# Kernel tuning notes

Measured on AMD Instinct MI355X. Metric: run time of the kernel, lower is better.

## Reference

```python
import jax, jax.numpy as jnp
import numpy as np

# MANO fingertip / palm prior vertex indices from contact_loss
_F1 = [697,698,699,700,712,713,714,715,737,738,739,740,741,743,744,745,746,748,749,750,753,754,755,756,757,758,759,760,761,762,763,764,765,766,767,768]
_F2 = [46,47,48,49,164,165,166,167,194,195,223,237,238,280,281,298,301,317,320,323,324,325,326,327,328,329,330,331,332,333,340,341,342,343,344,345,346,347,348,349,350,351,352,353,354,355]
_F3 = [356,357,358,359,375,376,386,387,396,397,402,403,413,429,433,434,435,436,437,438,439,440,441,442,443,444,452,453,454,455,456,459,460,461,462,463,464,465,466,467]
_F4 = [468,469,470,471,484,485,486,496,497,506,507,513,514,524,545,546,547,548,549,550,551,552,553,555,563,564,565,566,567,570,572,573,574,575,576,577,578]
_F5 = [580,581,582,583,600,601,602,614,615,624,625,630,631,641,663,664,665,666,667,668,670,672,680,681,682,683,684,686,687,688,689,690,691,692,693,694,695]
_F0 = [73,96,98,99,772,774,775,777]
PRIOR_IDX = np.array(_F1 + _F2 + _F3 + _F4 + _F5 + _F0, dtype=np.int32)

KL_COEF = 0.005
A_W, B_W, C_W, D_W, E_W = 1.0, 0.1, 1000.0, 10.0, 10.0  # init kwargs a..e


def _nn(src, trg):
    """Brute-force 1-NN: src [B,N1,3] -> trg [B,N2,3].
    Returns (sq_dist [B,N1], idx [B,N1], diff src-near [B,N1,3])."""
    d2 = (jnp.sum(src * src, -1)[:, :, None]
          + jnp.sum(trg * trg, -1)[:, None, :]
          - 2.0 * jnp.einsum('bnd,bmd->bnm', src, trg))  # [B,N1,N2]
    idx = jnp.argmin(d2, axis=-1)
    near = jnp.take_along_axis(trg, idx[:, :, None], axis=1)
    diff = src - near
    return jnp.sum(diff * diff, axis=-1), idx, diff


def _p2p_signed(x, y, x_normals):
    """point2point_signed(x, y, x_normals): signed dist y->x, unsigned x->y."""
    _, yidx, y2x = _nn(y, x)  # nearest x for each y
    y_nn_normal = jnp.take_along_axis(x_normals, yidx[:, :, None], axis=1)
    in_out = jnp.sign(jnp.sum(y_nn_normal * y2x, axis=-1))
    y2x_signed = jnp.sqrt(jnp.sum(y2x * y2x, axis=-1)) * in_out  # [B,P2]
    _, _, x2y = _nn(x, y)  # nearest y for each x
    x2y_dist = jnp.sqrt(jnp.sum(x2y * x2y, axis=-1))  # [B,P1]
    return y2x_signed, x2y_dist


def _forward(recon_xyz, gt_xyz, recon_normals, gt_normals, obj_xyz, mean, log_var, v_weights):
    B = recon_xyz.shape[0]
    f32 = recon_xyz.dtype
    # --- CVAE recon (L2) + KLD ---
    recon_loss = jnp.sum((recon_xyz - gt_xyz) ** 2) / B
    kld = -0.5 * jnp.sum(1.0 + log_var - mean ** 2 - jnp.exp(log_var)) / B * 10.0
    # --- obj -> hand NN (squared dists, pytorch3d knn_points convention) ---
    recon_d2, recon_idx, _ = _nn(obj_xyz, recon_xyz)  # [B,3000]
    gt_d2, _, _ = _nn(obj_xyz, gt_xyz)
    # --- contact map from GT NN dist thresholding ---
    cmap = jnp.sqrt(gt_d2) < 0.005  # [B,3000] bool
    # --- contact_loss: obj NN to prior (fingertip/palm) recon verts ---
    prior = recon_xyz[:, PRIOR_IDX, :]
    obj_cd, _, _ = _nn(obj_xyz, prior)
    n_pts = jnp.sum(cmap.astype(f32))
    contact = 3000.0 * jnp.where(n_pts > 0, jnp.sum(obj_cd * cmap) / (B * n_pts), 0.0)
    # --- CMap_consistency_loss ---
    recon_cmap = jnp.sqrt(recon_d2) < 0.005
    consistency = -5.0 * jnp.sum((recon_cmap & cmap).astype(f32)) / (n_pts + 1e-4)
    # --- inter_penetr_loss: interior obj points via NN-normal dot sign ---
    nn_hand = jnp.take_along_axis(recon_xyz, recon_idx[:, :, None], axis=1)
    nn_normal = jnp.take_along_axis(recon_normals, recon_idx[:, :, None], axis=1)
    interior = jnp.sum((nn_hand - obj_xyz) * nn_normal, axis=-1) > 0
    penetr = 100.0 * jnp.sum(recon_d2 * interior) / B
    # --- loss_cnet: signed chamfer consistency ---
    vw2 = v_weights ** (1.0 / 2.5)
    o2h, h2o = _p2p_signed(recon_xyz, obj_xyz, recon_normals)
    o2h_gt, h2o_gt = _p2p_signed(gt_xyz, obj_xyz, gt_normals)
    w_dist = (o2h_gt < 0.01) & (o2h_gt > -0.005)
    w_neg = o2h < 0.0
    w = jnp.where(w_neg, 1.5, jnp.where(w_dist, 1.0, 0.1))
    loss_h = 35.0 * (1.0 - KL_COEF) * jnp.mean(jnp.abs(jnp.abs(h2o) - jnp.abs(h2o_gt)) * vw2)
    loss_o = 30.0 * (1.0 - KL_COEF) * jnp.mean(jnp.abs(o2h - o2h_gt) * w)
    cnet = loss_h + loss_o
    return (A_W * recon_loss + B_W * kld + C_W * penetr
            + D_W * contact + E_W * consistency + cnet)


def setup_inputs() -> dict:
    key = jax.random.key(0)
    ks = jax.random.split(key, 8)
    B, NH, NO, Z = 32, 778, 3000, 64
    s = 0.05  # meter-scale point clouds so contact thresholds (5mm) are meaningful
    def unit(k, shape):
        v = jax.random.normal(k, shape, dtype=jnp.float32)
        return v / jnp.linalg.norm(v, axis=-1, keepdims=True)
    return {
        'recon_xyz': jax.random.normal(ks[0], (B, NH, 3), dtype=jnp.float32) * s,
        'gt_xyz': jax.random.normal(ks[1], (B, NH, 3), dtype=jnp.float32) * s,
        'recon_normals': unit(ks[2], (B, NH, 3)),
        'gt_normals': unit(ks[3], (B, NH, 3)),
        'obj_xyz': jax.random.normal(ks[4], (B, NO, 3), dtype=jnp.float32) * s,
        'mean': jax.random.normal(ks[5], (B, Z), dtype=jnp.float32),
        'log_var': jax.random.normal(ks[6], (B, Z), dtype=jnp.float32) * 0.1,
        'v_weights': jax.random.uniform(ks[7], (NH,), dtype=jnp.float32),
    }


def reference(recon_xyz, gt_xyz, recon_normals, gt_normals, obj_xyz, mean, log_var, v_weights):
    return _forward(recon_xyz, gt_xyz, recon_normals, gt_normals, obj_xyz, mean, log_var, v_weights)
```

## Files before the change

kernel.cpp:

```cpp
#include <hip/hip_runtime.h>
#include <math.h>


#define NB 32
#define NH 778
#define NO 3000
#define NZ 64
#define NP 204

#define P_OBJ 4
#define OBJ_PTS (256 * P_OBJ)
#define OBJ_TILES 3
#define JSPLIT 4
#define JCH 195
#define OC_NUM 12
#define OC_SIZE 250

#define OBJ_BLKS (NB * OBJ_TILES * JSPLIT)
#define HAND_BLKS (NB * OC_NUM)
#define FIN_OBJ_BLKS (NB * OBJ_TILES)
#define FIN_TAIL_BLKS ((NB * NH + 255) / 256)
#define FIN_BLKS (FIN_OBJ_BLKS + FIN_TAIL_BLKS)

typedef unsigned int uint32;
typedef unsigned long long ull;

__device__ __constant__ int c_prior[NP] = {
  697,698,699,700,712,713,714,715,737,738,739,740,741,743,744,745,746,748,749,750,
  753,754,755,756,757,758,759,760,761,762,763,764,765,766,767,768,
  46,47,48,49,164,165,166,167,194,195,223,237,238,280,281,298,301,317,320,323,
  324,325,326,327,328,329,330,331,332,333,340,341,342,343,344,345,346,347,348,349,
  350,351,352,353,354,355,
  356,357,358,359,375,376,386,387,396,397,402,403,413,429,433,434,435,436,437,438,
  439,440,441,442,443,444,452,453,454,455,456,459,460,461,462,463,464,465,466,467,
  468,469,470,471,484,485,486,496,497,506,507,513,514,524,545,546,547,548,549,550,
  551,552,553,555,563,564,565,566,567,570,572,573,574,575,576,577,578,
  580,581,582,583,600,601,602,614,615,624,625,630,631,641,663,664,665,666,667,668,
  670,672,680,681,682,683,684,686,687,688,689,690,691,692,693,694,695,
  73,96,98,99,772,774,775,777
};

__device__ inline float wave_sum(float v) {
  v += __shfl_down(v, 32);
  v += __shfl_down(v, 16);
  v += __shfl_down(v, 8);
  v += __shfl_down(v, 4);
  v += __shfl_down(v, 2);
  v += __shfl_down(v, 1);
  return v;
}

#define N_MINH (2 * NB * NH)
#define N_PACK (2 * NB * NO)

__global__ void init_kernel(float* accs, uint32* minH, ull* packO) {
  int t = blockIdx.x * blockDim.x + threadIdx.x;
  if (t < 9) accs[t] = 0.0f;
  if (t < N_MINH) minH[t] = 0x7F800000u;
  if (t < N_PACK) packO[t] = ~0ull;
}

__global__ __launch_bounds__(256) void mega1(
    const float* __restrict__ recon, const float* __restrict__ gt,
    const float* __restrict__ obj,
    uint32* __restrict__ minHR, uint32* __restrict__ minHG,
    ull* __restrict__ packR, ull* __restrict__ packG)
{
  const int bid = blockIdx.x;
  const int tid = threadIdx.x;

  if (bid < OBJ_BLKS) {
    __shared__ float4 sR[JCH];
    __shared__ float4 sG[JCH];
    const int b    = bid / (OBJ_TILES * JSPLIT);
    const int rem  = bid % (OBJ_TILES * JSPLIT);
    const int tile = rem / JSPLIT;
    const int half = rem % JSPLIT;
    const int jbase = half * JCH;
    const int jcnt = (NH - jbase < JCH) ? (NH - jbase) : JCH;

    for (int i = tid; i < jcnt; i += 256) {
      const float* p = recon + ((size_t)b * NH + jbase + i) * 3;
      float x = p[0], y = p[1], z = p[2];
      sR[i] = make_float4(x, y, z, x*x + y*y + z*z);
      const float* q = gt + ((size_t)b * NH + jbase + i) * 3;
      float gx = q[0], gy = q[1], gz = q[2];
      sG[i] = make_float4(gx, gy, gz, gx*gx + gy*gy + gz*gz);
    }
    __syncthreads();

    float nx[P_OBJ], ny[P_OBJ], nz[P_OBJ], o2v[P_OBJ];
    int ob[P_OBJ]; bool val[P_OBJ];
    #pragma unroll
    for (int m = 0; m < P_OBJ; ++m) {
      int o = tile * OBJ_PTS + m * 256 + tid;
      ob[m] = o; val[m] = (o < NO);
      float x = 0.f, y = 0.f, z = 0.f;
      if (val[m]) {
        const float* op = obj + ((size_t)b * NO + o) * 3;
        x = op[0]; y = op[1]; z = op[2];
      }
      nx[m] = -2.f * x; ny[m] = -2.f * y; nz[m] = -2.f * z;
      o2v[m] = x*x + y*y + z*z;
    }

    float bR[P_OBJ], bG[P_OBJ]; int iR[P_OBJ], iG[P_OBJ];
    #pragma unroll
    for (int m = 0; m < P_OBJ; ++m) { bR[m] = 3.4e38f; bG[m] = 3.4e38f; iR[m] = 0; iG[m] = 0; }

    #pragma unroll 2
    for (int i = 0; i < jcnt; ++i) {
      float4 h = sR[i];
      #pragma unroll
      for (int m = 0; m < P_OBJ; ++m) {
        float t = fmaf(nx[m], h.x, h.w);
        t = fmaf(ny[m], h.y, t);
        t = fmaf(nz[m], h.z, t);
        if (t < bR[m]) { bR[m] = t; iR[m] = jbase + i; }
      }
      float4 g = sG[i];
      #pragma unroll
      for (int m = 0; m < P_OBJ; ++m) {
        float u = fmaf(nx[m], g.x, g.w);
        u = fmaf(ny[m], g.y, u);
        u = fmaf(nz[m], g.z, u);
        if (u < bG[m]) { bG[m] = u; iG[m] = jbase + i; }
      }
    }

    #pragma unroll
    for (int m = 0; m < P_OBJ; ++m) {
      if (!val[m]) continue;
      const size_t base = (size_t)b * NO + ob[m];
      float d2R = fmaxf(bR[m] + o2v[m], 0.f);
      float d2G = fmaxf(bG[m] + o2v[m], 0.f);
      atomicMin(&packR[base], ((ull)__float_as_uint(d2R) << 32) | (uint32)iR[m]);
      atomicMin(&packG[base], ((ull)__float_as_uint(d2G) << 32) | (uint32)iG[m]);
    }
  } else {
    __shared__ float4 sO[OC_SIZE];
    const int bid2 = bid - OBJ_BLKS;
    const int oc = bid2 % OC_NUM;
    const int b  = bid2 / OC_NUM;

    const float* Ob = obj + ((size_t)b * NO + oc * OC_SIZE) * 3;
    for (int i = tid; i < OC_SIZE; i += 256) {
      float x = Ob[3*i], y = Ob[3*i+1], z = Ob[3*i+2];
      sO[i] = make_float4(x, y, z, x*x + y*y + z*z);
    }
    __syncthreads();

    float nrx[4], nry[4], nrz[4], r2v[4];
    float ngx[4], ngy[4], ngz[4], g2v[4];
    bool val[4];
    #pragma unroll
    for (int m = 0; m < 4; ++m) {
      int j = m * 256 + tid;
      val[m] = (j < NH);
      float rx = 0.f, ry = 0.f, rz = 0.f, gx = 0.f, gy = 0.f, gz = 0.f;
      if (val[m]) {
        const float* rp = recon + ((size_t)b * NH + j) * 3;
        const float* gp = gt    + ((size_t)b * NH + j) * 3;
        rx = rp[0]; ry = rp[1]; rz = rp[2];
        gx = gp[0]; gy = gp[1]; gz = gp[2];
      }
      nrx[m] = -2.f*rx; nry[m] = -2.f*ry; nrz[m] = -2.f*rz;
      ngx[m] = -2.f*gx; ngy[m] = -2.f*gy; ngz[m] = -2.f*gz;
      r2v[m] = rx*rx + ry*ry + rz*rz;
      g2v[m] = gx*gx + gy*gy + gz*gz;
    }

    float mR[4], mG[4];
    #pragma unroll
    for (int m = 0; m < 4; ++m) { mR[m] = 3.4e38f; mG[m] = 3.4e38f; }

    #pragma unroll 2
    for (int k = 0; k < OC_SIZE; ++k) {
      float4 o4 = sO[k];
      #pragma unroll
      for (int m = 0; m < 4; ++m) {
        float t = fmaf(nrx[m], o4.x, o4.w);
        t = fmaf(nry[m], o4.y, t);
        t = fmaf(nrz[m], o4.z, t);
        mR[m] = fminf(mR[m], t);
        float u = fmaf(ngx[m], o4.x, o4.w);
        u = fmaf(ngy[m], o4.y, u);
        u = fmaf(ngz[m], o4.z, u);
        mG[m] = fminf(mG[m], u);
      }
    }

    #pragma unroll
    for (int m = 0; m < 4; ++m) {
      if (!val[m]) continue;
      int j = m * 256 + tid;
      const int base = b * NH + j;
      float d2R = fmaxf(mR[m] + r2v[m], 0.f);
      float d2G = fmaxf(mG[m] + g2v[m], 0.f);
      atomicMin(&minHR[base], __float_as_uint(d2R));
      atomicMin(&minHG[base], __float_as_uint(d2G));
    }
  }
}

__global__ __launch_bounds__(256) void mega2(
    const float* __restrict__ recon, const float* __restrict__ gt,
    const float* __restrict__ rnorm, const float* __restrict__ gnorm,
    const float* __restrict__ obj,
    const float* __restrict__ mean, const float* __restrict__ logv,
    const float* __restrict__ vw,
    const uint32* __restrict__ minHR, const uint32* __restrict__ minHG,
    const ull* __restrict__ packR, const ull* __restrict__ packG,
    float* __restrict__ accs, float* __restrict__ out)
{
  __shared__ float4 sP[NP];
  __shared__ float red[4][5];
  const int bid = blockIdx.x;
  const int tid = threadIdx.x;
  const int lane = tid & 63, wv = tid >> 6;

  if (bid < FIN_OBJ_BLKS) {
    const int b = bid / OBJ_TILES;
    const int tile = bid % OBJ_TILES;
    if (tid < NP) {
      int j = c_prior[tid];
      const float* p = recon + ((size_t)b * NH + j) * 3;
      float x = p[0], y = p[1], z = p[2];
      sP[tid] = make_float4(x, y, z, x*x + y*y + z*z);
    }
    __syncthreads();

    float nx[P_OBJ], ny[P_OBJ], nz[P_OBJ], o2v[P_OBJ];
    float oxv[P_OBJ], oyv[P_OBJ], ozv[P_OBJ];
    int ob[P_OBJ]; bool val[P_OBJ];
    #pragma unroll
    for (int m = 0; m < P_OBJ; ++m) {
      int o = tile * OBJ_PTS + m * 256 + tid;
      ob[m] = o; val[m] = (o < NO);
      float x = 0.f, y = 0.f, z = 0.f;
      if (val[m]) {
        const float* op = obj + ((size_t)b * NO + o) * 3;
        x = op[0]; y = op[1]; z = op[2];
      }
      oxv[m] = x; oyv[m] = y; ozv[m] = z;
      nx[m] = -2.f * x; ny[m] = -2.f * y; nz[m] = -2.f * z;
      o2v[m] = x*x + y*y + z*z;
    }

    float bP[P_OBJ];
    #pragma unroll
    for (int m = 0; m < P_OBJ; ++m) bP[m] = 3.4e38f;
    #pragma unroll 2
    for (int k = 0; k < NP; ++k) {
      float4 h = sP[k];
      #pragma unroll
      for (int m = 0; m < P_OBJ; ++m) {
        float t = fmaf(nx[m], h.x, h.w);
        t = fmaf(ny[m], h.y, t);
        t = fmaf(nz[m], h.z, t);
        bP[m] = fminf(bP[m], t);
      }
    }

    float penetr = 0.f, nptsv = 0.f, contactv = 0.f, consistv = 0.f, lossov = 0.f;
    #pragma unroll
    for (int m = 0; m < P_OBJ; ++m) {
      if (!val[m]) continue;
      const size_t base = (size_t)b * NO + ob[m];
      ull pR = packR[base], pG = packG[base];
      float d2R = __uint_as_float((uint32)(pR >> 32));
      float d2G = __uint_as_float((uint32)(pG >> 32));
      int idxR = (int)(uint32)pR, idxG = (int)(uint32)pG;
      float d2P = fmaxf(bP[m] + o2v[m], 0.f);

      const float* hR = recon + ((size_t)b * NH + idxR) * 3;
      const float* nR = rnorm + ((size_t)b * NH + idxR) * 3;
      float dotR = (oxv[m] - hR[0]) * nR[0] + (oyv[m] - hR[1]) * nR[1] + (ozv[m] - hR[2]) * nR[2];
      const float* hG = gt + ((size_t)b * NH + idxG) * 3;
      const float* nG = gnorm + ((size_t)b * NH + idxG) * 3;
      float dotG = (oxv[m] - hG[0]) * nG[0] + (oyv[m] - hG[1]) * nG[1] + (ozv[m] - hG[2]) * nG[2];

      float sgnR = (dotR > 0.f) ? 1.f : ((dotR < 0.f) ? -1.f : 0.f);
      float sgnG = (dotG > 0.f) ? 1.f : ((dotG < 0.f) ? -1.f : 0.f);
      float sR_ = sqrtf(d2R), sG_ = sqrtf(d2G);
      float o2h = sR_ * sgnR, o2hg = sG_ * sgnG;

      bool interior = dotR < 0.f;
      bool cmap = sG_ < 0.005f;
      bool rcmap = sR_ < 0.005f;

      penetr   += interior ? d2R : 0.f;
      nptsv    += cmap ? 1.f : 0.f;
      contactv += cmap ? d2P : 0.f;
      consistv += (cmap && rcmap) ? 1.f : 0.f;
      float w = (o2h < 0.f) ? 1.5f
              : (((o2hg < 0.01f) && (o2hg > -0.005f)) ? 1.f : 0.1f);
      lossov += fabsf(o2h - o2hg) * w;
    }

    float vals[5] = {penetr, nptsv, contactv, consistv, lossov};
    for (int q = 0; q < 5; ++q) {
      float s = wave_sum(vals[q]);
      if (lane == 0) red[wv][q] = s;
    }
    __syncthreads();
    if (tid < 5) {
      float s = red[0][tid] + red[1][tid] + red[2][tid] + red[3][tid];
      atomicAdd(&accs[tid], s);
    }
  } else {
    const int t = (bid - FIN_OBJ_BLKS) * 256 + tid;
    float lossh = 0.f, rsum = 0.f, ksum = 0.f;
    if (t < NB * NH) {
      const float* rp = recon + (size_t)t * 3;
      const float* gp = gt + (size_t)t * 3;
      float d0 = rp[0] - gp[0], d1 = rp[1] - gp[1], d2 = rp[2] - gp[2];
      rsum = d0*d0 + d1*d1 + d2*d2;
      int j = t % NH;
      float h2o  = sqrtf(__uint_as_float(minHR[t]));
      float h2og = sqrtf(__uint_as_float(minHG[t]));
      lossh = fabsf(h2o - h2og) * powf(vw[j], 0.4f);
    }
    if (t < NB * NZ) {
      float m = mean[t], lv = logv[t];
      ksum = 1.f + lv - m * m - expf(lv);
    }
    float vals[3] = {lossh, rsum, ksum};
    for (int q = 0; q < 3; ++q) {
      float s = wave_sum(vals[q]);
      if (lane == 0) red[wv][q] = s;
    }
    __syncthreads();
    if (tid < 3) {
      float s = red[0][tid] + red[1][tid] + red[2][tid] + red[3][tid];
      atomicAdd(&accs[5 + tid], s);
    }
  }

  __syncthreads();
  if (tid == 0) {
    __threadfence();
    int* cnt = (int*)(accs + 8);
    int old = atomicAdd(cnt, 1);
    if (old == FIN_BLKS - 1) {
      float a[8];
      for (int q = 0; q < 8; ++q) a[q] = atomicAdd(&accs[q], 0.0f);
      const float recon_loss = a[6] / (float)NB;
      const float kld = -0.5f * a[7] / (float)NB * 10.f;
      const float penetr = 100.f * a[0] / (float)NB;
      const float npts = a[1];
      const float contact = (npts > 0.f) ? (3000.f * a[2] / ((float)NB * npts)) : 0.f;
      const float consistency = -5.f * a[3] / (npts + 0.0001f);
      const float lossh = 35.f * (1.f - 0.005f) * (a[5] / (float)(NB * NH));
      const float losso = 30.f * (1.f - 0.005f) * (a[4] / (float)(NB * NO));
      out[0] = recon_loss + 0.1f * kld + 1000.f * penetr + 10.f * contact
             + 10.f * consistency + lossh + losso;
    }
  }
}

#define FB_TILES 12
__global__ __launch_bounds__(256) void obj_mono(
    const float* __restrict__ recon, const float* __restrict__ gt,
    const float* __restrict__ rnorm, const float* __restrict__ gnorm,
    const float* __restrict__ obj, float* __restrict__ accs)
{
  __shared__ float4 sR[NH];
  __shared__ float4 sG[NH];
  __shared__ float red[4][5];
  const int b = blockIdx.x / FB_TILES;
  const int tile = blockIdx.x % FB_TILES;
  const int tid = threadIdx.x;

  for (int i = tid; i < NH; i += 256) {
    const float* p = recon + ((size_t)b * NH + i) * 3;
    float x = p[0], y = p[1], z = p[2];
    sR[i] = make_float4(x, y, z, x*x + y*y + z*z);
    const float* q = gt + ((size_t)b * NH + i) * 3;
    float gx = q[0], gy = q[1], gz = q[2];
    sG[i] = make_float4(gx, gy, gz, gx*gx + gy*gy + gz*gz);
  }
  __syncthreads();

  const int o = tile * 256 + tid;
  float penetr = 0.f, nptsv = 0.f, contactv = 0.f, consistv = 0.f, lossov = 0.f;
  if (o < NO) {
    const float* op = obj + ((size_t)b * NO + o) * 3;
    const float ox = op[0], oy = op[1], oz = op[2];
    const float nx = -2.f * ox, ny = -2.f * oy, nz = -2.f * oz;
    const float o2 = ox*ox + oy*oy + oz*oz;
    float bR = 3.4e38f, bG = 3.4e38f;
    int iR = 0, iG = 0;
    for (int i = 0; i < NH; ++i) {
      float4 h = sR[i];
      float t = fmaf(nx, h.x, h.w); t = fmaf(ny, h.y, t); t = fmaf(nz, h.z, t);
      if (t < bR) { bR = t; iR = i; }
      float4 g = sG[i];
      float u = fmaf(nx, g.x, g.w); u = fmaf(ny, g.y, u); u = fmaf(nz, g.z, u);
      if (u < bG) { bG = u; iG = i; }
    }
    float bP = 3.4e38f;
    for (int k = 0; k < NP; ++k) {
      float4 h = sR[c_prior[k]];
      float t = fmaf(nx, h.x, h.w); t = fmaf(ny, h.y, t); t = fmaf(nz, h.z, t);
      bP = fminf(bP, t);
    }
    float d2R = fmaxf(bR + o2, 0.f);
    float d2G = fmaxf(bG + o2, 0.f);
    float d2P = fmaxf(bP + o2, 0.f);
    float4 hR = sR[iR];
    const float* nR = rnorm + ((size_t)b * NH + iR) * 3;
    float dotR = (ox - hR.x) * nR[0] + (oy - hR.y) * nR[1] + (oz - hR.z) * nR[2];
    float4 hG = sG[iG];
    const float* nG = gnorm + ((size_t)b * NH + iG) * 3;
    float dotG = (ox - hG.x) * nG[0] + (oy - hG.y) * nG[1] + (oz - hG.z) * nG[2];
    float sgnR = (dotR > 0.f) ? 1.f : ((dotR < 0.f) ? -1.f : 0.f);
    float sgnG = (dotG > 0.f) ? 1.f : ((dotG < 0.f) ? -1.f : 0.f);
    float sR_ = sqrtf(d2R), sG_ = sqrtf(d2G);
    float o2h = sR_ * sgnR, o2hg = sG_ * sgnG;
    bool interior = dotR < 0.f;
    bool cmap = sG_ < 0.005f, rcmap = sR_ < 0.005f;
    penetr = interior ? d2R : 0.f;
    nptsv = cmap ? 1.f : 0.f;
    contactv = cmap ? d2P : 0.f;
    consistv = (cmap && rcmap) ? 1.f : 0.f;
    float w = (o2h < 0.f) ? 1.5f : (((o2hg < 0.01f) && (o2hg > -0.005f)) ? 1.f : 0.1f);
    lossov = fabsf(o2h - o2hg) * w;
  }
  float vals[5] = {penetr, nptsv, contactv, consistv, lossov};
  const int lane = tid & 63, wv = tid >> 6;
  for (int q = 0; q < 5; ++q) {
    float s = wave_sum(vals[q]);
    if (lane == 0) red[wv][q] = s;
  }
  __syncthreads();
  if (tid < 5) {
    float s = red[0][tid] + red[1][tid] + red[2][tid] + red[3][tid];
    atomicAdd(&accs[tid], s);
  }
}

__global__ __launch_bounds__(256) void hand_full(
    const float* __restrict__ recon, const float* __restrict__ gt,
    const float* __restrict__ obj, const float* __restrict__ vw,
    float* __restrict__ accs)
{
  __shared__ float4 sO[500];
  __shared__ float red[4];
  const int b = blockIdx.x >> 2;
  const int j = ((blockIdx.x & 3) << 8) + threadIdx.x;
  const bool valid = j < NH;
  float rx = 0, ry = 0, rz = 0, gx = 0, gy = 0, gz = 0;
  if (valid) {
    const float* rp = recon + ((size_t)b * NH + j) * 3;
    const float* gp = gt + ((size_t)b * NH + j) * 3;
    rx = rp[0]; ry = rp[1]; rz = rp[2];
    gx = gp[0]; gy = gp[1]; gz = gp[2];
  }
  const float nrx = -2.f*rx, nry = -2.f*ry, nrz = -2.f*rz;
  const float ngx = -2.f*gx, ngy = -2.f*gy, ngz = -2.f*gz;
  const float r2 = rx*rx + ry*ry + rz*rz, g2 = gx*gx + gy*gy + gz*gz;
  float mR = 3.4e38f, mG = 3.4e38f;
  for (int oc = 0; oc < 6; ++oc) {
    __syncthreads();
    const float* Ob = obj + ((size_t)b * NO + oc * 500) * 3;
    for (int i = threadIdx.x; i < 500; i += 256) {
      float x = Ob[3*i], y = Ob[3*i+1], z = Ob[3*i+2];
      sO[i] = make_float4(x, y, z, x*x + y*y + z*z);
    }
    __syncthreads();
    if (valid) {
      for (int k = 0; k < 500; ++k) {
        float4 o4 = sO[k];
        float t = fmaf(nrx, o4.x, o4.w); t = fmaf(nry, o4.y, t); t = fmaf(nrz, o4.z, t);
        mR = fminf(mR, t);
        float u = fmaf(ngx, o4.x, o4.w); u = fmaf(ngy, o4.y, u); u = fmaf(ngz, o4.z, u);
        mG = fminf(mG, u);
      }
    }
  }
  float lossh = valid ? fabsf(sqrtf(fmaxf(mR + r2, 0.f)) - sqrtf(fmaxf(mG + g2, 0.f)))
                        * powf(vw[j], 0.4f) : 0.f;
  const int lane = threadIdx.x & 63, wv = threadIdx.x >> 6;
  float s = wave_sum(lossh);
  if (lane == 0) red[wv] = s;
  __syncthreads();
  if (threadIdx.x == 0) atomicAdd(&accs[5], red[0] + red[1] + red[2] + red[3]);
}

__global__ __launch_bounds__(256) void tail_nomins(
    const float* __restrict__ recon, const float* __restrict__ gt,
    const float* __restrict__ mean, const float* __restrict__ logv,
    float* __restrict__ accs)
{
  __shared__ float red[4][2];
  const int t = blockIdx.x * 256 + threadIdx.x;
  float rsum = 0.f, ksum = 0.f;
  if (t < NB * NH) {
    const float* rp = recon + (size_t)t * 3;
    const float* gp = gt + (size_t)t * 3;
    float d0 = rp[0] - gp[0], d1 = rp[1] - gp[1], d2 = rp[2] - gp[2];
    rsum = d0*d0 + d1*d1 + d2*d2;
  }
  if (t < NB * NZ) {
    float m = mean[t], lv = logv[t];
    ksum = 1.f + lv - m * m - expf(lv);
  }
  float vals[2] = {rsum, ksum};
  const int lane = threadIdx.x & 63, wv = threadIdx.x >> 6;
  for (int q = 0; q < 2; ++q) {
    float s = wave_sum(vals[q]);
    if (lane == 0) red[wv][q] = s;
  }
  __syncthreads();
  if (threadIdx.x < 2) {
    float s = red[0][threadIdx.x] + red[1][threadIdx.x] + red[2][threadIdx.x] + red[3][threadIdx.x];
    atomicAdd(&accs[6 + threadIdx.x], s);
  }
}

__global__ void init_small(float* accs) {
  int t = threadIdx.x;
  if (t < 8) accs[t] = 0.0f;
}

__global__ void final_fb(const float* __restrict__ a, float* __restrict__ out) {
  const float recon_loss = a[6] / (float)NB;
  const float kld = -0.5f * a[7] / (float)NB * 10.f;
  const float penetr = 100.f * a[0] / (float)NB;
  const float npts = a[1];
  const float contact = (npts > 0.f) ? (3000.f * a[2] / ((float)NB * npts)) : 0.f;
  const float consistency = -5.f * a[3] / (npts + 0.0001f);
  const float lossh = 35.f * (1.f - 0.005f) * (a[5] / (float)(NB * NH));
  const float losso = 30.f * (1.f - 0.005f) * (a[4] / (float)(NB * NO));
  out[0] = recon_loss + 0.1f * kld + 1000.f * penetr + 10.f * contact
         + 10.f * consistency + lossh + losso;
}

extern "C" void kernel_launch(void* const* d_in, const int* in_sizes, int n_in,
                              void* d_out, int out_size, void* d_ws, size_t ws_size,
                              hipStream_t stream) {
  const float* recon = (const float*)d_in[0];
  const float* gt    = (const float*)d_in[1];
  const float* rnorm = (const float*)d_in[2];
  const float* gnorm = (const float*)d_in[3];
  const float* obj   = (const float*)d_in[4];
  const float* mean  = (const float*)d_in[5];
  const float* logv  = (const float*)d_in[6];
  const float* vw    = (const float*)d_in[7];
  float* out = (float*)d_out;

  float* accs = (float*)d_ws;
  uint32* minH = (uint32*)(accs + 16);
  ull* packO = (ull*)(minH + N_MINH);
  const size_t needed = 16 * sizeof(float) + (size_t)N_MINH * 4 + (size_t)N_PACK * 8;

  if (ws_size >= needed) {
    {
      int blocks = (N_PACK + 255) / 256;
      init_kernel<<<blocks, 256, 0, stream>>>(accs, minH, packO);
    }
    mega1<<<OBJ_BLKS + HAND_BLKS, 256, 0, stream>>>(
        recon, gt, obj, minH, minH + NB * NH, packO, packO + NB * NO);
    mega2<<<FIN_BLKS, 256, 0, stream>>>(
        recon, gt, rnorm, gnorm, obj, mean, logv, vw,
        minH, minH + NB * NH, packO, packO + NB * NO, accs, out);
  } else {
    init_small<<<1, 64, 0, stream>>>(accs);
    obj_mono<<<NB * FB_TILES, 256, 0, stream>>>(recon, gt, rnorm, gnorm, obj, accs);
    hand_full<<<NB * 4, 256, 0, stream>>>(recon, gt, obj, vw, accs);
    tail_nomins<<<(NB * NH + 255) / 256, 256, 0, stream>>>(recon, gt, mean, logv, accs);
    final_fb<<<1, 1, 0, stream>>>(accs, out);
  }
}
```

Measured before the change: 129.5 us.

## Fuse NN and finalize kernels via last-block counters and packed 32-bit keys

Merges the two main kernels into one. Arrival counters let the last split block for each object tile, and the last hand-chunk block for each batch, run the finalization work inline, and a global counter triggers the final combine. The argmin index is packed into the low 10 mantissa bits of the float distance, so the inner loop drops its compare-branch for fminf and the atomics become 32-bit instead of 64-bit. This removes one kernel launch and the 64-bit packing, at the cost of slightly perturbed distances (truncated mantissa) that could change near-threshold decisions or tie-breaking.

```diff
diff --git a/kernel.cpp b/kernel.cpp
--- a/kernel.cpp
+++ b/kernel.cpp
@@ -9,21 +9,21 @@
 #define NP 204
 
 #define P_OBJ 4
-#define OBJ_PTS (256 * P_OBJ)
+#define OBJ_PTS 1024
 #define OBJ_TILES 3
 #define JSPLIT 4
 #define JCH 195
-#define OC_NUM 12
-#define OC_SIZE 250
-
+#define HC 12
+#define HCS 250
 #define OBJ_BLKS (NB * OBJ_TILES * JSPLIT)
-#define HAND_BLKS (NB * OC_NUM)
-#define FIN_OBJ_BLKS (NB * OBJ_TILES)
-#define FIN_TAIL_BLKS ((NB * NH + 255) / 256)
-#define FIN_BLKS (FIN_OBJ_BLKS + FIN_TAIL_BLKS)
+#define HAND_BLKS (NB * HC)
+#define NKEY (NB * NO)
+#define NHT  (NB * NH)
+#define NCNT (1 + NB * OBJ_TILES + NB)
+#define N_CONTRIB (NB * OBJ_TILES + NB)
+#define NSENT (2 * NKEY + 2 * NHT)
 
 typedef unsigned int uint32;
-typedef unsigned long long ull;
 
 __device__ __constant__ int c_prior[NP] = {
   697,698,699,700,712,713,714,715,737,738,739,740,741,743,744,745,746,748,749,750,
@@ -50,46 +50,86 @@
   return v;
 }
 
-#define N_MINH (2 * NB * NH)
-#define N_PACK (2 * NB * NO)
-
-__global__ void init_kernel(float* accs, uint32* minH, ull* packO) {
-  int t = blockIdx.x * blockDim.x + threadIdx.x;
-  if (t < 9) accs[t] = 0.0f;
-  if (t < N_MINH) minH[t] = 0x7F800000u;
-  if (t < N_PACK) packO[t] = ~0ull;
-}
-
-__global__ __launch_bounds__(256) void mega1(
+__device__ inline float packkey(float t, int j) {
+  return __uint_as_float((__float_as_uint(t) & 0xFFFFFC00u) | (uint32)j);
+}
+__device__ inline uint32 mono(float f) {
+  uint32 b = __float_as_uint(f);
+  return b ^ (uint32)(((int)b >> 31) | 0x80000000);
+}
+__device__ inline uint32 unmono(uint32 u) {
+  return u ^ ((u & 0x80000000u) ? 0x80000000u : 0xFFFFFFFFu);
+}
+__device__ inline float aread(float* p) {
+  return atomicAdd(p, 0.0f);
+}
+__device__ inline uint32 areadu(uint32* p) {
+  return atomicOr(p, 0u);
+}
+
+__global__ void init_k(float* __restrict__ accs, int* __restrict__ cnts,
+                       uint32* __restrict__ sent) {
+  int t = blockIdx.x * 256 + threadIdx.x;
+  if (t < 16) accs[t] = 0.0f;
+  if (t < NCNT) cnts[t] = 0;
+  for (int i = t; i < NSENT; i += gridDim.x * 256) sent[i] = 0xFFFFFFFFu;
+}
+
+__device__ inline void final_combine(float* accs, float* out) {
+  float a[8];
+  #pragma unroll
+  for (int q = 0; q < 8; ++q) a[q] = aread(&accs[q]);
+  const float recon_loss = a[6] / (float)NB;
+  const float kld = -0.5f * a[7] / (float)NB * 10.f;
+  const float penetr = 100.f * a[0] / (float)NB;
+  const float npts = a[1];
+  const float contact = (npts > 0.f) ? (3000.f * a[2] / ((float)NB * npts)) : 0.f;
+  const float consistency = -5.f * a[3] / (npts + 0.0001f);
+  const float lossh = 35.f * (1.f - 0.005f) * (a[5] / (float)(NB * NH));
+  const float losso = 30.f * (1.f - 0.005f) * (a[4] / (float)(NB * NO));
+  out[0] = recon_loss + 0.1f * kld + 1000.f * penetr + 10.f * contact
+         + 10.f * consistency + lossh + losso;
+}
+
+__global__ __launch_bounds__(256) void mega(
     const float* __restrict__ recon, const float* __restrict__ gt,
+    const float* __restrict__ rnorm, const float* __restrict__ gnorm,
     const float* __restrict__ obj,
+    const float* __restrict__ mean, const float* __restrict__ logv,
+    const float* __restrict__ vw,
+    uint32* __restrict__ keyR, uint32* __restrict__ keyG,
     uint32* __restrict__ minHR, uint32* __restrict__ minHG,
-    ull* __restrict__ packR, ull* __restrict__ packG)
+    float* __restrict__ accs, int* __restrict__ gcnt,
+    int* __restrict__ cntObj, int* __restrict__ cntHand,
+    float* __restrict__ out)
 {
+  __shared__ float4 shA[HCS];
+  __shared__ float4 shB[NP];
+  __shared__ float red[4][5];
+  __shared__ int flag;
   const int bid = blockIdx.x;
   const int tid = threadIdx.x;
+  const int lane = tid & 63, wv = tid >> 6;
 
   if (bid < OBJ_BLKS) {
-    __shared__ float4 sR[JCH];
-    __shared__ float4 sG[JCH];
-    const int b    = bid / (OBJ_TILES * JSPLIT);
-    const int rem  = bid % (OBJ_TILES * JSPLIT);
-    const int tile = rem / JSPLIT;
-    const int half = rem % JSPLIT;
-    const int jbase = half * JCH;
-    const int jcnt = (NH - jbase < JCH) ? (NH - jbase) : JCH;
+    const int b     = bid / (OBJ_TILES * JSPLIT);
+    const int rem   = bid % (OBJ_TILES * JSPLIT);
+    const int tile  = rem / JSPLIT;
+    const int split = rem % JSPLIT;
+    const int jbase = split * JCH;
+    const int jcnt  = (NH - jbase < JCH) ? (NH - jbase) : JCH;
 
     for (int i = tid; i < jcnt; i += 256) {
       const float* p = recon + ((size_t)b * NH + jbase + i) * 3;
       float x = p[0], y = p[1], z = p[2];
-      sR[i] = make_float4(x, y, z, x*x + y*y + z*z);
+      shA[i] = make_float4(x, y, z, x*x + y*y + z*z);
       const float* q = gt + ((size_t)b * NH + jbase + i) * 3;
       float gx = q[0], gy = q[1], gz = q[2];
-      sG[i] = make_float4(gx, gy, gz, gx*gx + gy*gy + gz*gz);
-    }
-    __syncthreads();
-
-    float nx[P_OBJ], ny[P_OBJ], nz[P_OBJ], o2v[P_OBJ];
+      shB[i] = make_float4(gx, gy, gz, gx*gx + gy*gy + gz*gz);
+    }
+    __syncthreads();
+
+    float nx[P_OBJ], ny[P_OBJ], nz[P_OBJ];
     int ob[P_OBJ]; bool val[P_OBJ];
     #pragma unroll
     for (int m = 0; m < P_OBJ; ++m) {
@@ -101,57 +141,140 @@
         x = op[0]; y = op[1]; z = op[2];
       }
       nx[m] = -2.f * x; ny[m] = -2.f * y; nz[m] = -2.f * z;
-      o2v[m] = x*x + y*y + z*z;
-    }
-
-    float bR[P_OBJ], bG[P_OBJ]; int iR[P_OBJ], iG[P_OBJ];
-    #pragma unroll
-    for (int m = 0; m < P_OBJ; ++m) { bR[m] = 3.4e38f; bG[m] = 3.4e38f; iR[m] = 0; iG[m] = 0; }
-
-    #pragma unroll 2
-    for (int i = 0; i < jcnt; ++i) {
-      float4 h = sR[i];
+    }
+
+    float bR[P_OBJ], bG[P_OBJ];
+    #pragma unroll
+    for (int m = 0; m < P_OBJ; ++m) { bR[m] = 3.4e38f; bG[m] = 3.4e38f; }
+
+    int i = 0;
+    for (; i + 1 < jcnt; i += 2) {
+      float4 h0 = shA[i], h1 = shA[i + 1];
       #pragma unroll
       for (int m = 0; m < P_OBJ; ++m) {
-        float t = fmaf(nx[m], h.x, h.w);
-        t = fmaf(ny[m], h.y, t);
-        t = fmaf(nz[m], h.z, t);
-        if (t < bR[m]) { bR[m] = t; iR[m] = jbase + i; }
-      }
-      float4 g = sG[i];
+        float t0 = fmaf(nx[m], h0.x, h0.w); t0 = fmaf(ny[m], h0.y, t0); t0 = fmaf(nz[m], h0.z, t0);
+        float t1 = fmaf(nx[m], h1.x, h1.w); t1 = fmaf(ny[m], h1.y, t1); t1 = fmaf(nz[m], h1.z, t1);
+        bR[m] = fminf(bR[m], fminf(packkey(t0, jbase + i), packkey(t1, jbase + i + 1)));
+      }
+      float4 g0 = shB[i], g1 = shB[i + 1];
       #pragma unroll
       for (int m = 0; m < P_OBJ; ++m) {
-        float u = fmaf(nx[m], g.x, g.w);
-        u = fmaf(ny[m], g.y, u);
-        u = fmaf(nz[m], g.z, u);
-        if (u < bG[m]) { bG[m] = u; iG[m] = jbase + i; }
+        float t0 = fmaf(nx[m], g0.x, g0.w); t0 = fmaf(ny[m], g0.y, t0); t0 = fmaf(nz[m], g0.z, t0);
+        float t1 = fmaf(nx[m], g1.x, g1.w); t1 = fmaf(ny[m], g1.y, t1); t1 = fmaf(nz[m], g1.z, t1);
+        bG[m] = fminf(bG[m], fminf(packkey(t0, jbase + i), packkey(t1, jbase + i + 1)));
+      }
+    }
+    if (i < jcnt) {
+      float4 h0 = shA[i];
+      float4 g0 = shB[i];
+      #pragma unroll
+      for (int m = 0; m < P_OBJ; ++m) {
+        float t0 = fmaf(nx[m], h0.x, h0.w); t0 = fmaf(ny[m], h0.y, t0); t0 = fmaf(nz[m], h0.z, t0);
+        bR[m] = fminf(bR[m], packkey(t0, jbase + i));
+        float u0 = fmaf(nx[m], g0.x, g0.w); u0 = fmaf(ny[m], g0.y, u0); u0 = fmaf(nz[m], g0.z, u0);
+        bG[m] = fminf(bG[m], packkey(u0, jbase + i));
       }
     }
 
     #pragma unroll
     for (int m = 0; m < P_OBJ; ++m) {
       if (!val[m]) continue;
-      const size_t base = (size_t)b * NO + ob[m];
-      float d2R = fmaxf(bR[m] + o2v[m], 0.f);
-      float d2G = fmaxf(bG[m] + o2v[m], 0.f);
-      atomicMin(&packR[base], ((ull)__float_as_uint(d2R) << 32) | (uint32)iR[m]);
-      atomicMin(&packG[base], ((ull)__float_as_uint(d2G) << 32) | (uint32)iG[m]);
+      const uint32 base = (uint32)(b * NO + ob[m]);
+      atomicMin(&keyR[base], mono(bR[m]));
+      atomicMin(&keyG[base], mono(bG[m]));
+    }
+    __threadfence();
+    __syncthreads();
+    if (tid == 0)
+      flag = (atomicAdd(&cntObj[b * OBJ_TILES + tile], 1) == JSPLIT - 1) ? 1 : 0;
+    __syncthreads();
+    if (!flag) return;
+
+    if (tid < NP) {
+      int j = c_prior[tid];
+      const float* p = recon + ((size_t)b * NH + j) * 3;
+      float x = p[0], y = p[1], z = p[2];
+      shB[tid] = make_float4(x, y, z, x*x + y*y + z*z);
+    }
+    __syncthreads();
+    if (tid == 0) __threadfence();
+    float penetr = 0.f, nptsv = 0.f, contactv = 0.f, consistv = 0.f, lossov = 0.f;
+    #pragma unroll
+    for (int m = 0; m < P_OBJ; ++m) {
+      if (!val[m]) continue;
+      const float ox = -0.5f * nx[m], oy = -0.5f * ny[m], oz = -0.5f * nz[m];
+      const float o2 = ox*ox + oy*oy + oz*oz;
+      const uint32 base = (uint32)(b * NO + ob[m]);
+      uint32 kRb = unmono(areadu(&keyR[base]));
+      uint32 kGb = unmono(areadu(&keyG[base]));
+      int idxR = (int)(kRb & 0x3FFu), idxG = (int)(kGb & 0x3FFu);
+      float d2R = fmaxf(__uint_as_float(kRb & 0xFFFFFC00u) + o2, 0.f);
+      float d2G = fmaxf(__uint_as_float(kGb & 0xFFFFFC00u) + o2, 0.f);
+
+      float bP = 3.4e38f;
+      for (int k = 0; k < NP; k += 2) {
+        float4 h0 = shB[k], h1 = shB[k + 1];
+        float t0 = fmaf(nx[m], h0.x, h0.w); t0 = fmaf(ny[m], h0.y, t0); t0 = fmaf(nz[m], h0.z, t0);
+        float t1 = fmaf(nx[m], h1.x, h1.w); t1 = fmaf(ny[m], h1.y, t1); t1 = fmaf(nz[m], h1.z, t1);
+        bP = fminf(bP, fminf(t0, t1));
+      }
+      float d2P = fmaxf(bP + o2, 0.f);
+
+      const float* hR = recon + ((size_t)b * NH + idxR) * 3;
+      const float* nR = rnorm + ((size_t)b * NH + idxR) * 3;
+      float dotR = (ox - hR[0]) * nR[0] + (oy - hR[1]) * nR[1] + (oz - hR[2]) * nR[2];
+      const float* hG = gt + ((size_t)b * NH + idxG) * 3;
+      const float* nG = gnorm + ((size_t)b * NH + idxG) * 3;
+      float dotG = (ox - hG[0]) * nG[0] + (oy - hG[1]) * nG[1] + (oz - hG[2]) * nG[2];
+
+      float sgnR = (dotR > 0.f) ? 1.f : ((dotR < 0.f) ? -1.f : 0.f);
+      float sgnG = (dotG > 0.f) ? 1.f : ((dotG < 0.f) ? -1.f : 0.f);
+      float sR_ = sqrtf(d2R), sG_ = sqrtf(d2G);
+      float o2h = sR_ * sgnR, o2hg = sG_ * sgnG;
+
+      bool interior = dotR < 0.f;
+      bool cmap = sG_ < 0.005f;
+      bool rcmap = sR_ < 0.005f;
+
+      penetr   += interior ? d2R : 0.f;
+      nptsv    += cmap ? 1.f : 0.f;
+      contactv += cmap ? d2P : 0.f;
+      consistv += (cmap && rcmap) ? 1.f : 0.f;
+      float w = (o2h < 0.f) ? 1.5f
+              : (((o2hg < 0.01f) && (o2hg > -0.005f)) ? 1.f : 0.1f);
+      lossov += fabsf(o2h - o2hg) * w;
+    }
+
+    float vals[5] = {penetr, nptsv, contactv, consistv, lossov};
+    #pragma unroll
+    for (int q = 0; q < 5; ++q) {
+      float s = wave_sum(vals[q]);
+      if (lane == 0) red[wv][q] = s;
+    }
+    __syncthreads();
+    if (tid < 5) {
+      float s = red[0][tid] + red[1][tid] + red[2][tid] + red[3][tid];
+      atomicAdd(&accs[tid], s);
+    }
+    __threadfence();
+    __syncthreads();
+    if (tid == 0) {
+      if (atomicAdd(gcnt, 1) == N_CONTRIB - 1) final_combine(accs, out);
     }
   } else {
-    __shared__ float4 sO[OC_SIZE];
     const int bid2 = bid - OBJ_BLKS;
-    const int oc = bid2 % OC_NUM;
-    const int b  = bid2 / OC_NUM;
-
-    const float* Ob = obj + ((size_t)b * NO + oc * OC_SIZE) * 3;
-    for (int i = tid; i < OC_SIZE; i += 256) {
-      float x = Ob[3*i], y = Ob[3*i+1], z = Ob[3*i+2];
-      sO[i] = make_float4(x, y, z, x*x + y*y + z*z);
-    }
-    __syncthreads();
-
-    float nrx[4], nry[4], nrz[4], r2v[4];
-    float ngx[4], ngy[4], ngz[4], g2v[4];
+    const int oc = bid2 % HC;
+    const int b  = bid2 / HC;
+
+    const float* Ob = obj + ((size_t)b * NO + oc * HCS) * 3;
+    for (int i2 = tid; i2 < HCS; i2 += 256) {
+      float x = Ob[3*i2], y = Ob[3*i2+1], z = Ob[3*i2+2];
+      shA[i2] = make_float4(x, y, z, x*x + y*y + z*z);
+    }
+    __syncthreads();
+
+    float nrx[4], nry[4], nrz[4];
+    float ngx[4], ngy[4], ngz[4];
     bool val[4];
     #pragma unroll
     for (int m = 0; m < 4; ++m) {
@@ -166,27 +289,22 @@
       }
       nrx[m] = -2.f*rx; nry[m] = -2.f*ry; nrz[m] = -2.f*rz;
       ngx[m] = -2.f*gx; ngy[m] = -2.f*gy; ngz[m] = -2.f*gz;
-      r2v[m] = rx*rx + ry*ry + rz*rz;
-      g2v[m] = gx*gx + gy*gy + gz*gz;
     }
 
     float mR[4], mG[4];
     #pragma unroll
     for (int m = 0; m < 4; ++m) { mR[m] = 3.4e38f; mG[m] = 3.4e38f; }
 
-    #pragma unroll 2
-    for (int k = 0; k < OC_SIZE; ++k) {
-      float4 o4 = sO[k];
+    for (int k = 0; k < HCS; k += 2) {
+      float4 o0 = shA[k], o1 = shA[k + 1];
       #pragma unroll
       for (int m = 0; m < 4; ++m) {
-        float t = fmaf(nrx[m], o4.x, o4.w);
-        t = fmaf(nry[m], o4.y, t);
-        t = fmaf(nrz[m], o4.z, t);
-        mR[m] = fminf(mR[m], t);
-        float u = fmaf(ngx[m], o4.x, o4.w);
-        u = fmaf(ngy[m], o4.y, u);
-        u = fmaf(ngz[m], o4.z, u);
-        mG[m] = fminf(mG[m], u);
+        float t0 = fmaf(nrx[m], o0.x, o0.w); t0 = fmaf(nry[m], o0.y, t0); t0 = fmaf(nrz[m], o0.z, t0);
+        float t1 = fmaf(nrx[m], o1.x, o1.w); t1 = fmaf(nry[m], o1.y, t1); t1 = fmaf(nrz[m], o1.z, t1);
+        mR[m] = fminf(mR[m], fminf(t0, t1));
+        float u0 = fmaf(ngx[m], o0.x, o0.w); u0 = fmaf(ngy[m], o0.y, u0); u0 = fmaf(ngz[m], o0.z, u0);
+        float u1 = fmaf(ngx[m], o1.x, o1.w); u1 = fmaf(ngy[m], o1.y, u1); u1 = fmaf(ngz[m], o1.z, u1);
+        mG[m] = fminf(mG[m], fminf(u0, u1));
       }
     }
 
@@ -194,138 +312,44 @@
     for (int m = 0; m < 4; ++m) {
       if (!val[m]) continue;
       int j = m * 256 + tid;
-      const int base = b * NH + j;
-      float d2R = fmaxf(mR[m] + r2v[m], 0.f);
-      float d2G = fmaxf(mG[m] + g2v[m], 0.f);
-      atomicMin(&minHR[base], __float_as_uint(d2R));
-      atomicMin(&minHG[base], __float_as_uint(d2G));
-    }
-  }
-}
-
-__global__ __launch_bounds__(256) void mega2(
-    const float* __restrict__ recon, const float* __restrict__ gt,
-    const float* __restrict__ rnorm, const float* __restrict__ gnorm,
-    const float* __restrict__ obj,
-    const float* __restrict__ mean, const float* __restrict__ logv,
-    const float* __restrict__ vw,
-    const uint32* __restrict__ minHR, const uint32* __restrict__ minHG,
-    const ull* __restrict__ packR, const ull* __restrict__ packG,
-    float* __restrict__ accs, float* __restrict__ out)
-{
-  __shared__ float4 sP[NP];
-  __shared__ float red[4][5];
-  const int bid = blockIdx.x;
-  const int tid = threadIdx.x;
-  const int lane = tid & 63, wv = tid >> 6;
-
-  if (bid < FIN_OBJ_BLKS) {
-    const int b = bid / OBJ_TILES;
-    const int tile = bid % OBJ_TILES;
-    if (tid < NP) {
-      int j = c_prior[tid];
-      const float* p = recon + ((size_t)b * NH + j) * 3;
-      float x = p[0], y = p[1], z = p[2];
-      sP[tid] = make_float4(x, y, z, x*x + y*y + z*z);
-    }
-    __syncthreads();
-
-    float nx[P_OBJ], ny[P_OBJ], nz[P_OBJ], o2v[P_OBJ];
-    float oxv[P_OBJ], oyv[P_OBJ], ozv[P_OBJ];
-    int ob[P_OBJ]; bool val[P_OBJ];
-    #pragma unroll
-    for (int m = 0; m < P_OBJ; ++m) {
-      int o = tile * OBJ_PTS + m * 256 + tid;
-      ob[m] = o; val[m] = (o < NO);
-      float x = 0.f, y = 0.f, z = 0.f;
-      if (val[m]) {
-        const float* op = obj + ((size_t)b * NO + o) * 3;
-        x = op[0]; y = op[1]; z = op[2];
-      }
-      oxv[m] = x; oyv[m] = y; ozv[m] = z;
-      nx[m] = -2.f * x; ny[m] = -2.f * y; nz[m] = -2.f * z;
-      o2v[m] = x*x + y*y + z*z;
-    }
-
-    float bP[P_OBJ];
-    #pragma unroll
-    for (int m = 0; m < P_OBJ; ++m) bP[m] = 3.4e38f;
-    #pragma unroll 2
-    for (int k = 0; k < NP; ++k) {
-      float4 h = sP[k];
-      #pragma unroll
-      for (int m = 0; m < P_OBJ; ++m) {
-        float t = fmaf(nx[m], h.x, h.w);
-        t = fmaf(ny[m], h.y, t);
-        t = fmaf(nz[m], h.z, t);
-        bP[m] = fminf(bP[m], t);
-      }
-    }
-
-    float penetr = 0.f, nptsv = 0.f, contactv = 0.f, consistv = 0.f, lossov = 0.f;
-    #pragma unroll
-    for (int m = 0; m < P_OBJ; ++m) {
-      if (!val[m]) continue;
-      const size_t base = (size_t)b * NO + ob[m];
-      ull pR = packR[base], pG = packG[base];
-      float d2R = __uint_as_float((uint32)(pR >> 32));
-      float d2G = __uint_as_float((uint32)(pG >> 32));
-      int idxR = (int)(uint32)pR, idxG = (int)(uint32)pG;
-      float d2P = fmaxf(bP[m] + o2v[m], 0.f);
-
-      const float* hR = recon + ((size_t)b * NH + idxR) * 3;
-      const float* nR = rnorm + ((size_t)b * NH + idxR) * 3;
-      float dotR = (oxv[m] - hR[0]) * nR[0] + (oyv[m] - hR[1]) * nR[1] + (ozv[m] - hR[2]) * nR[2];
-      const float* hG = gt + ((size_t)b * NH + idxG) * 3;
-      const float* nG = gnorm + ((size_t)b * NH + idxG) * 3;
-      float dotG = (oxv[m] - hG[0]) * nG[0] + (oyv[m] - hG[1]) * nG[1] + (ozv[m] - hG[2]) * nG[2];
-
-      float sgnR = (dotR > 0.f) ? 1.f : ((dotR < 0.f) ? -1.f : 0.f);
-      float sgnG = (dotG > 0.f) ? 1.f : ((dotG < 0.f) ? -1.f : 0.f);
-      float sR_ = sqrtf(d2R), sG_ = sqrtf(d2G);
-      float o2h = sR_ * sgnR, o2hg = sG_ * sgnG;
-
-      bool interior = dotR < 0.f;
-      bool cmap = sG_ < 0.005f;
-      bool rcmap = sR_ < 0.005f;
-
-      penetr   += interior ? d2R : 0.f;
-      nptsv    += cmap ? 1.f : 0.f;
-      contactv += cmap ? d2P : 0.f;
-      consistv += (cmap && rcmap) ? 1.f : 0.f;
-      float w = (o2h < 0.f) ? 1.5f
-              : (((o2hg < 0.01f) && (o2hg > -0.005f)) ? 1.f : 0.1f);
-      lossov += fabsf(o2h - o2hg) * w;
-    }
-
-    float vals[5] = {penetr, nptsv, contactv, consistv, lossov};
-    for (int q = 0; q < 5; ++q) {
-      float s = wave_sum(vals[q]);
-      if (lane == 0) red[wv][q] = s;
-    }
-    __syncthreads();
-    if (tid < 5) {
-      float s = red[0][tid] + red[1][tid] + red[2][tid] + red[3][tid];
-      atomicAdd(&accs[tid], s);
-    }
-  } else {
-    const int t = (bid - FIN_OBJ_BLKS) * 256 + tid;
+      const uint32 idx = (uint32)(b * NH + j);
+      atomicMin(&minHR[idx], mono(mR[m]));
+      atomicMin(&minHG[idx], mono(mG[m]));
+    }
+    __threadfence();
+    __syncthreads();
+    if (tid == 0)
+      flag = (atomicAdd(&cntHand[b], 1) == HC - 1) ? 1 : 0;
+    __syncthreads();
+    if (!flag) return;
+
+    if (tid == 0) __threadfence();
     float lossh = 0.f, rsum = 0.f, ksum = 0.f;
-    if (t < NB * NH) {
-      const float* rp = recon + (size_t)t * 3;
-      const float* gp = gt + (size_t)t * 3;
-      float d0 = rp[0] - gp[0], d1 = rp[1] - gp[1], d2 = rp[2] - gp[2];
-      rsum = d0*d0 + d1*d1 + d2*d2;
-      int j = t % NH;
-      float h2o  = sqrtf(__uint_as_float(minHR[t]));
-      float h2og = sqrtf(__uint_as_float(minHG[t]));
-      lossh = fabsf(h2o - h2og) * powf(vw[j], 0.4f);
-    }
-    if (t < NB * NZ) {
-      float m = mean[t], lv = logv[t];
-      ksum = 1.f + lv - m * m - expf(lv);
+    #pragma unroll
+    for (int m = 0; m < 4; ++m) {
+      int j = m * 256 + tid;
+      if (j >= NH) continue;
+      const float* rp = recon + ((size_t)b * NH + j) * 3;
+      const float* gp = gt    + ((size_t)b * NH + j) * 3;
+      float rx = rp[0], ry = rp[1], rz = rp[2];
+      float gx = gp[0], gy = gp[1], gz = gp[2];
+      float d0 = rx - gx, d1 = ry - gy, d2 = rz - gz;
+      rsum += d0*d0 + d1*d1 + d2*d2;
+
+      float tR = __uint_as_float(unmono(areadu(&minHR[b * NH + j])));
+      float tG = __uint_as_float(unmono(areadu(&minHG[b * NH + j])));
+      float r2 = rx*rx + ry*ry + rz*rz;
+      float g2 = gx*gx + gy*gy + gz*gz;
+      float d2Rh = fmaxf(tR + r2, 0.f);
+      float d2Gh = fmaxf(tG + g2, 0.f);
+      lossh += fabsf(sqrtf(d2Rh) - sqrtf(d2Gh)) * powf(vw[j], 0.4f);
+    }
+    if (tid < NZ) {
+      float mm = mean[b * NZ + tid], lv = logv[b * NZ + tid];
+      ksum = 1.f + lv - mm * mm - expf(lv);
     }
     float vals[3] = {lossh, rsum, ksum};
+    #pragma unroll
     for (int q = 0; q < 3; ++q) {
       float s = wave_sum(vals[q]);
       if (lane == 0) red[wv][q] = s;
@@ -335,31 +359,14 @@
       float s = red[0][tid] + red[1][tid] + red[2][tid] + red[3][tid];
       atomicAdd(&accs[5 + tid], s);
     }
-  }
-
-  __syncthreads();
-  if (tid == 0) {
     __threadfence();
-    int* cnt = (int*)(accs + 8);
-    int old = atomicAdd(cnt, 1);
-    if (old == FIN_BLKS - 1) {
-      float a[8];
-      for (int q = 0; q < 8; ++q) a[q] = atomicAdd(&accs[q], 0.0f);
-      const float recon_loss = a[6] / (float)NB;
-      const float kld = -0.5f * a[7] / (float)NB * 10.f;
-      const float penetr = 100.f * a[0] / (float)NB;
-      const float npts = a[1];
-      const float contact = (npts > 0.f) ? (3000.f * a[2] / ((float)NB * npts)) : 0.f;
-      const float consistency = -5.f * a[3] / (npts + 0.0001f);
-      const float lossh = 35.f * (1.f - 0.005f) * (a[5] / (float)(NB * NH));
-      const float losso = 30.f * (1.f - 0.005f) * (a[4] / (float)(NB * NO));
-      out[0] = recon_loss + 0.1f * kld + 1000.f * penetr + 10.f * contact
-             + 10.f * consistency + lossh + losso;
-    }
-  }
-}
-
-#define FB_TILES 12
+    __syncthreads();
+    if (tid == 0) {
+      if (atomicAdd(gcnt, 1) == N_CONTRIB - 1) final_combine(accs, out);
+    }
+  }
+}
+
 __global__ __launch_bounds__(256) void obj_mono(
     const float* __restrict__ recon, const float* __restrict__ gt,
     const float* __restrict__ rnorm, const float* __restrict__ gnorm,
@@ -368,10 +375,9 @@
   __shared__ float4 sR[NH];
   __shared__ float4 sG[NH];
   __shared__ float red[4][5];
-  const int b = blockIdx.x / FB_TILES;
-  const int tile = blockIdx.x % FB_TILES;
+  const int b = blockIdx.x / 12;
+  const int tile = blockIdx.x % 12;
   const int tid = threadIdx.x;
-
   for (int i = tid; i < NH; i += 256) {
     const float* p = recon + ((size_t)b * NH + i) * 3;
     float x = p[0], y = p[1], z = p[2];
@@ -381,16 +387,14 @@
     sG[i] = make_float4(gx, gy, gz, gx*gx + gy*gy + gz*gz);
   }
   __syncthreads();
-
   const int o = tile * 256 + tid;
   float penetr = 0.f, nptsv = 0.f, contactv = 0.f, consistv = 0.f, lossov = 0.f;
   if (o < NO) {
     const float* op = obj + ((size_t)b * NO + o) * 3;
     const float ox = op[0], oy = op[1], oz = op[2];
-    const float nx = -2.f * ox, ny = -2.f * oy, nz = -2.f * oz;
+    const float nx = -2.f*ox, ny = -2.f*oy, nz = -2.f*oz;
     const float o2 = ox*ox + oy*oy + oz*oz;
-    float bR = 3.4e38f, bG = 3.4e38f;
-    int iR = 0, iG = 0;
+    float bR = 3.4e38f, bG = 3.4e38f; int iR = 0, iG = 0;
     for (int i = 0; i < NH; ++i) {
       float4 h = sR[i];
       float t = fmaf(nx, h.x, h.w); t = fmaf(ny, h.y, t); t = fmaf(nz, h.z, t);
@@ -410,14 +414,14 @@
     float d2P = fmaxf(bP + o2, 0.f);
     float4 hR = sR[iR];
     const float* nR = rnorm + ((size_t)b * NH + iR) * 3;
-    float dotR = (ox - hR.x) * nR[0] + (oy - hR.y) * nR[1] + (oz - hR.z) * nR[2];
+    float dotR = (ox-hR.x)*nR[0] + (oy-hR.y)*nR[1] + (oz-hR.z)*nR[2];
     float4 hG = sG[iG];
     const float* nG = gnorm + ((size_t)b * NH + iG) * 3;
-    float dotG = (ox - hG.x) * nG[0] + (oy - hG.y) * nG[1] + (oz - hG.z) * nG[2];
+    float dotG = (ox-hG.x)*nG[0] + (oy-hG.y)*nG[1] + (oz-hG.z)*nG[2];
     float sgnR = (dotR > 0.f) ? 1.f : ((dotR < 0.f) ? -1.f : 0.f);
     float sgnG = (dotG > 0.f) ? 1.f : ((dotG < 0.f) ? -1.f : 0.f);
     float sR_ = sqrtf(d2R), sG_ = sqrtf(d2G);
-    float o2h = sR_ * sgnR, o2hg = sG_ * sgnG;
+    float o2h = sR_*sgnR, o2hg = sG_*sgnG;
     bool interior = dotR < 0.f;
     bool cmap = sG_ < 0.005f, rcmap = sR_ < 0.005f;
     penetr = interior ? d2R : 0.f;
@@ -450,16 +454,15 @@
   const int b = blockIdx.x >> 2;
   const int j = ((blockIdx.x & 3) << 8) + threadIdx.x;
   const bool valid = j < NH;
-  float rx = 0, ry = 0, rz = 0, gx = 0, gy = 0, gz = 0;
+  float rx=0,ry=0,rz=0,gx=0,gy=0,gz=0;
   if (valid) {
     const float* rp = recon + ((size_t)b * NH + j) * 3;
     const float* gp = gt + ((size_t)b * NH + j) * 3;
-    rx = rp[0]; ry = rp[1]; rz = rp[2];
-    gx = gp[0]; gy = gp[1]; gz = gp[2];
-  }
-  const float nrx = -2.f*rx, nry = -2.f*ry, nrz = -2.f*rz;
-  const float ngx = -2.f*gx, ngy = -2.f*gy, ngz = -2.f*gz;
-  const float r2 = rx*rx + ry*ry + rz*rz, g2 = gx*gx + gy*gy + gz*gz;
+    rx=rp[0];ry=rp[1];rz=rp[2]; gx=gp[0];gy=gp[1];gz=gp[2];
+  }
+  const float nrx=-2.f*rx, nry=-2.f*ry, nrz=-2.f*rz;
+  const float ngx=-2.f*gx, ngy=-2.f*gy, ngz=-2.f*gz;
+  const float r2 = rx*rx+ry*ry+rz*rz, g2 = gx*gx+gy*gy+gz*gz;
   float mR = 3.4e38f, mG = 3.4e38f;
   for (int oc = 0; oc < 6; ++oc) {
     __syncthreads();
@@ -472,20 +475,19 @@
     if (valid) {
       for (int k = 0; k < 500; ++k) {
         float4 o4 = sO[k];
-        float t = fmaf(nrx, o4.x, o4.w); t = fmaf(nry, o4.y, t); t = fmaf(nrz, o4.z, t);
+        float t = fmaf(nrx,o4.x,o4.w); t = fmaf(nry,o4.y,t); t = fmaf(nrz,o4.z,t);
         mR = fminf(mR, t);
-        float u = fmaf(ngx, o4.x, o4.w); u = fmaf(ngy, o4.y, u); u = fmaf(ngz, o4.z, u);
+        float u = fmaf(ngx,o4.x,o4.w); u = fmaf(ngy,o4.y,u); u = fmaf(ngz,o4.z,u);
         mG = fminf(mG, u);
       }
     }
   }
-  float lossh = valid ? fabsf(sqrtf(fmaxf(mR + r2, 0.f)) - sqrtf(fmaxf(mG + g2, 0.f)))
-                        * powf(vw[j], 0.4f) : 0.f;
+  float lossh = valid ? fabsf(sqrtf(fmaxf(mR+r2,0.f)) - sqrtf(fmaxf(mG+g2,0.f))) * powf(vw[j], 0.4f) : 0.f;
   const int lane = threadIdx.x & 63, wv = threadIdx.x >> 6;
   float s = wave_sum(lossh);
   if (lane == 0) red[wv] = s;
   __syncthreads();
-  if (threadIdx.x == 0) atomicAdd(&accs[5], red[0] + red[1] + red[2] + red[3]);
+  if (threadIdx.x == 0) atomicAdd(&accs[5], red[0]+red[1]+red[2]+red[3]);
 }
 
 __global__ __launch_bounds__(256) void tail_nomins(
@@ -499,12 +501,12 @@
   if (t < NB * NH) {
     const float* rp = recon + (size_t)t * 3;
     const float* gp = gt + (size_t)t * 3;
-    float d0 = rp[0] - gp[0], d1 = rp[1] - gp[1], d2 = rp[2] - gp[2];
+    float d0 = rp[0]-gp[0], d1 = rp[1]-gp[1], d2 = rp[2]-gp[2];
     rsum = d0*d0 + d1*d1 + d2*d2;
   }
   if (t < NB * NZ) {
     float m = mean[t], lv = logv[t];
-    ksum = 1.f + lv - m * m - expf(lv);
+    ksum = 1.f + lv - m*m - expf(lv);
   }
   float vals[2] = {rsum, ksum};
   const int lane = threadIdx.x & 63, wv = threadIdx.x >> 6;
@@ -533,8 +535,7 @@
   const float consistency = -5.f * a[3] / (npts + 0.0001f);
   const float lossh = 35.f * (1.f - 0.005f) * (a[5] / (float)(NB * NH));
   const float losso = 30.f * (1.f - 0.005f) * (a[4] / (float)(NB * NO));
-  out[0] = recon_loss + 0.1f * kld + 1000.f * penetr + 10.f * contact
-         + 10.f * consistency + lossh + losso;
+  out[0] = recon_loss + 0.1f*kld + 1000.f*penetr + 10.f*contact + 10.f*consistency + lossh + losso;
 }
 
 extern "C" void kernel_launch(void* const* d_in, const int* in_sizes, int n_in,
@@ -551,23 +552,23 @@
   float* out = (float*)d_out;
 
   float* accs = (float*)d_ws;
-  uint32* minH = (uint32*)(accs + 16);
-  ull* packO = (ull*)(minH + N_MINH);
-  const size_t needed = 16 * sizeof(float) + (size_t)N_MINH * 4 + (size_t)N_PACK * 8;
-
-  if (ws_size >= needed) {
-    {
-      int blocks = (N_PACK + 255) / 256;
-      init_kernel<<<blocks, 256, 0, stream>>>(accs, minH, packO);
-    }
-    mega1<<<OBJ_BLKS + HAND_BLKS, 256, 0, stream>>>(
-        recon, gt, obj, minH, minH + NB * NH, packO, packO + NB * NO);
-    mega2<<<FIN_BLKS, 256, 0, stream>>>(
+  int* gcnt = (int*)((char*)d_ws + 64);
+  int* cntObj = gcnt + 1;
+  int* cntHand = cntObj + NB * OBJ_TILES;
+  uint32* keyR = (uint32*)((char*)d_ws + 1024);
+  uint32* keyG = keyR + NKEY;
+  uint32* minHR = keyG + NKEY;
+  uint32* minHG = minHR + NHT;
+  const size_t neededA = 1024 + (size_t)NSENT * 4;
+
+  if (ws_size >= neededA) {
+    init_k<<<120, 256, 0, stream>>>(accs, gcnt, keyR);
+    mega<<<OBJ_BLKS + HAND_BLKS, 256, 0, stream>>>(
         recon, gt, rnorm, gnorm, obj, mean, logv, vw,
-        minH, minH + NB * NH, packO, packO + NB * NO, accs, out);
+        keyR, keyG, minHR, minHG, accs, gcnt, cntObj, cntHand, out);
   } else {
     init_small<<<1, 64, 0, stream>>>(accs);
-    obj_mono<<<NB * FB_TILES, 256, 0, stream>>>(recon, gt, rnorm, gnorm, obj, accs);
+    obj_mono<<<NB * 12, 256, 0, stream>>>(recon, gt, rnorm, gnorm, obj, accs);
     hand_full<<<NB * 4, 256, 0, stream>>>(recon, gt, obj, vw, accs);
     tail_nomins<<<(NB * NH + 255) / 256, 256, 0, stream>>>(recon, gt, mean, logv, accs);
     final_fb<<<1, 1, 0, stream>>>(accs, out);
```

After: 181.6 us. 1.4x slower.
